# Performance work log

Measured on AMD Instinct MI355X. Metric: run time of the kernel, lower is better.

## Reference

```python
import jax, jax.numpy as jnp
import numpy as np

B, N, C = 4, 4096, 1024
NUM_HEADS = 16
HEAD_DIM = C // NUM_HEADS


def setup_inputs() -> dict:
    key = jax.random.key(0)
    k1, k2, k3, k4 = jax.random.split(key, 4)
    s_in = 1.0 / np.sqrt(C)
    return {
        "x": jax.random.normal(k1, (B, N, C), dtype=jnp.float32),
        "H": 64,
        "W": 64,
        "Wqkv": jax.random.normal(k2, (3 * C, C), dtype=jnp.float32) * s_in,
        "Wproj": jax.random.normal(k3, (C, C), dtype=jnp.float32) * s_in,
        "bproj": jnp.zeros((C,), dtype=jnp.float32),
        "alpha": jnp.ones((NUM_HEADS,), dtype=jnp.float32),
    }


def reference(x, H, W, Wqkv, Wproj, bproj, alpha):
    Bb, Nn, Cc = x.shape
    h, d = NUM_HEADS, HEAD_DIM
    # qkv: [B, N, 3C] -> [3, B, h, N, d]
    qkv = jnp.einsum('bnc,oc->bno', x, Wqkv)
    qkv = qkv.reshape(Bb, Nn, 3, h, d).transpose(2, 0, 3, 1, 4)
    q, k, v = qkv[0], qkv[1], qkv[2]  # each [B, h, N, d]
    # channel attention: contract over tokens N -> [B, h, d, d]
    attn = jnp.einsum('bhnd,bhne->bhde', k, q) / alpha[None, :, None, None]
    attn = jax.nn.softmax(attn, axis=-1)
    # (dropout is identity in eval/reference mode)
    # head_out: [B, h, d, N] -> transpose -> [B, N, h, d] -> concat heads
    out = jnp.einsum('bhde,bhne->bhdn', attn, v)
    out = out.transpose(0, 3, 1, 2).reshape(Bb, Nn, Cc)
    return jnp.einsum('bnc,oc->bno', out, Wproj) + bproj
```

## Files before the change

### kernel.cpp

```cpp
#include <hip/hip_runtime.h>
#include <hip/hip_bf16.h>
#include <cstdint>
#include <cstddef>

typedef unsigned short u16;
typedef __bf16 bf16x8 __attribute__((ext_vector_type(8)));
typedef float f32x4 __attribute__((ext_vector_type(4)));
typedef unsigned short u16x4 __attribute__((ext_vector_type(4)));
typedef unsigned short u16x8 __attribute__((ext_vector_type(8)));

#define AS1(p) ((__attribute__((address_space(1))) void*)(p))
#define AS3(p) ((__attribute__((address_space(3))) void*)(p))

__device__ __forceinline__ float bf2f(u16 u) {
  unsigned v = ((unsigned)u) << 16; float f; __builtin_memcpy(&f, &v, 4); return f;
}
__device__ __forceinline__ u16 f2bf(float f) {
  unsigned u; __builtin_memcpy(&u, &f, 4);
  u += 0x7FFFu + ((u >> 16) & 1u);
  return (u16)(u >> 16);
}

__global__ __launch_bounds__(256) void convert_kernel(const float* __restrict__ src,
                                                      u16* __restrict__ dst, int n4) {
  int i = blockIdx.x * blockDim.x + threadIdx.x;
  int stride = gridDim.x * blockDim.x;
  for (; i < n4; i += stride) {
    float4 v = ((const float4*)src)[i];
    u16x4 o;
    o.x = f2bf(v.x); o.y = f2bf(v.y); o.z = f2bf(v.z); o.w = f2bf(v.w);
    ((u16x4*)dst)[i] = o;
  }
}

__global__ __launch_bounds__(256) void convert_split_kernel(const float* __restrict__ src,
                                                            u16* __restrict__ hi,
                                                            u16* __restrict__ lo, int n4) {
  int i = blockIdx.x * blockDim.x + threadIdx.x;
  int stride = gridDim.x * blockDim.x;
  for (; i < n4; i += stride) {
    float4 v = ((const float4*)src)[i];
    u16x4 oh, ol;
    oh.x = f2bf(v.x); ol.x = f2bf(v.x - bf2f(oh.x));
    oh.y = f2bf(v.y); ol.y = f2bf(v.y - bf2f(oh.y));
    oh.z = f2bf(v.z); ol.z = f2bf(v.z - bf2f(oh.z));
    oh.w = f2bf(v.w); ol.w = f2bf(v.w - bf2f(oh.w));
    ((u16x4*)hi)[i] = oh;
    ((u16x4*)lo)[i] = ol;
  }
}

__global__ __launch_bounds__(256) void transpose_split_kernel(const float* __restrict__ x,
                                                              u16* __restrict__ Xb,
                                                              u16* __restrict__ XThi,
                                                              u16* __restrict__ XTlo) {
  __shared__ u16 lhi[64 * 72];
  __shared__ u16 llo[64 * 72];
  const int t  = threadIdx.x;
  const int nT = blockIdx.x, cT = blockIdx.y, b = blockIdx.z;
  const size_t xbase = ((size_t)b * 4096 + nT * 64) * 1024 + cT * 64;
  const int c4 = (t & 15) * 4;
  const int r0 = t >> 4;
  const int rot_w = (t & 3) << 4;
#pragma unroll
  for (int j = 0; j < 4; ++j) {
    int r = r0 + j * 16;
    float4 v = *(const float4*)(x + xbase + (size_t)r * 1024 + c4);
    u16x4 hi;
    hi.x = f2bf(v.x); hi.y = f2bf(v.y); hi.z = f2bf(v.z); hi.w = f2bf(v.w);
    *(u16x4*)(Xb + xbase + (size_t)r * 1024 + c4) = hi;
    u16 lo[4];
    lo[0] = f2bf(v.x - bf2f(hi.x)); lo[1] = f2bf(v.y - bf2f(hi.y));
    lo[2] = f2bf(v.z - bf2f(hi.z)); lo[3] = f2bf(v.w - bf2f(hi.w));
    u16 hia[4] = { hi.x, hi.y, hi.z, hi.w };
    const int rs = r ^ rot_w;
#pragma unroll
    for (int i = 0; i < 4; ++i) {
      lhi[(c4 + i) * 72 + rs] = hia[i];
      llo[(c4 + i) * 72 + rs] = lo[i];
    }
  }
  __syncthreads();
  const int c  = t >> 2;
  const int n0 = (t & 3) * 16;
  const int rot_r = ((t >> 4) & 3) << 4;
  const int nA = n0 ^ rot_r;
  const size_t tbase = ((size_t)b * 1024 + cT * 64 + c) * 4096 + nT * 64 + n0;
  *(u16x8*)(XThi + tbase)     = *(const u16x8*)(lhi + c * 72 + nA);
  *(u16x8*)(XThi + tbase + 8) = *(const u16x8*)(lhi + c * 72 + nA + 8);
  *(u16x8*)(XTlo + tbase)     = *(const u16x8*)(llo + c * 72 + nA);
  *(u16x8*)(XTlo + tbase + 8) = *(const u16x8*)(llo + c * 72 + nA + 8);
}

template<bool OUT_BF16, bool HAS_BIAS>
__global__ __launch_bounds__(512, 2) void gemm_pipe(const u16* __restrict__ A,
                                                    const u16* __restrict__ B,
                                                    void* __restrict__ Cv,
                                                    const float* __restrict__ bias,
                                                    int M, int N, int K,
                                                    size_t sA, size_t sB, size_t sC) {
  __shared__ __align__(16) u16 lds[4][2][8192];
  const int tid  = threadIdx.x;
  const int lane = tid & 63;
  const int wave = tid >> 6;
  const int wm = wave >> 2, wn = wave & 3;
  const int rowTile = blockIdx.x * 256;
  const int colTile = blockIdx.y * 256;
  A += (size_t)blockIdx.z * sA;
  B += (size_t)blockIdx.z * sB;

  size_t srcA[2], srcB[2];
  int ldsOff[2];
#pragma unroll
  for (int j = 0; j < 2; ++j) {
    const int L = j * 512 + tid;
    const int sr = L >> 3;
    const int slot = (L & 7) ^ (sr & 7);
    const int r  = (sr << 1) | (slot >> 2);
    const int kq = slot & 3;
    srcA[j] = (size_t)(rowTile + r) * K + kq * 8;
    srcB[j] = (size_t)(colTile + r) * K + kq * 8;
    ldsOff[j] = (j * 512 + (tid & 448)) * 16;
  }

  const int m15 = lane & 15, kq4 = lane >> 4;
  const int r0a = wm * 128 + m15, sa0 = r0a >> 1;
  const int idxA0 = sa0 * 64 + (((((r0a & 1) << 2) | kq4)) ^ (sa0 & 7)) * 8;
  const int r0b = wn * 64 + m15, sb0 = r0b >> 1;
  const int idxB0 = sb0 * 64 + (((((r0b & 1) << 2) | kq4)) ^ (sb0 & 7)) * 8;

  const int NT = K >> 5;

  auto stageA = [&](int tt) {
    char* d = (char*)&lds[tt & 3][0][0];
    const int kt = tt << 5;
#pragma unroll
    for (int j = 0; j < 2; ++j)
      __builtin_amdgcn_global_load_lds(AS1(A + srcA[j] + kt), AS3(d + ldsOff[j]), 16, 0, 0);
  };
  auto stageB = [&](int tt) {
    char* d = (char*)&lds[tt & 3][1][0];
    const int kt = tt << 5;
#pragma unroll
    for (int j = 0; j < 2; ++j)
      __builtin_amdgcn_global_load_lds(AS1(B + srcB[j] + kt), AS3(d + ldsOff[j]), 16, 0, 0);
  };

  stageA(0); stageB(0);
  if (NT > 1) { stageA(1); stageB(1); }
  if (NT > 2) { stageA(2); stageB(2); }
  if (NT > 2) asm volatile("s_waitcnt vmcnt(8)" ::: "memory");
  else        asm volatile("s_waitcnt vmcnt(0)" ::: "memory");
  __builtin_amdgcn_sched_barrier(0);
  __builtin_amdgcn_s_barrier();
  __builtin_amdgcn_sched_barrier(0);

  f32x4 acc[8][4] = {};
  for (int t = 0; t < NT; ++t) {
    const u16* bufA = &lds[t & 3][0][0];
    const u16* bufB = &lds[t & 3][1][0];
    bf16x8 a[8], bfr[4];
#pragma unroll
    for (int ni = 0; ni < 4; ++ni) bfr[ni] = *(const bf16x8*)(bufB + idxB0 + ni * 512);
#pragma unroll
    for (int mi = 0; mi < 4; ++mi) a[mi] = *(const bf16x8*)(bufA + idxA0 + mi * 512);
    if (t + 3 < NT) stageA(t + 3);
    __builtin_amdgcn_sched_barrier(0);
    __builtin_amdgcn_s_barrier();
    __builtin_amdgcn_sched_barrier(0);
    __builtin_amdgcn_s_setprio(1);
#pragma unroll
    for (int mi = 0; mi < 4; ++mi)
#pragma unroll
      for (int ni = 0; ni < 4; ++ni)
        acc[mi][ni] = __builtin_amdgcn_mfma_f32_16x16x32_bf16(a[mi], bfr[ni], acc[mi][ni], 0, 0, 0);
    __builtin_amdgcn_s_setprio(0);
    __builtin_amdgcn_sched_barrier(0);
    __builtin_amdgcn_s_barrier();
    __builtin_amdgcn_sched_barrier(0);
#pragma unroll
    for (int mi = 4; mi < 8; ++mi) a[mi] = *(const bf16x8*)(bufA + idxA0 + mi * 512);
    if (t + 3 < NT) stageB(t + 3);
    __builtin_amdgcn_sched_barrier(0);
    __builtin_amdgcn_s_barrier();
    __builtin_amdgcn_sched_barrier(0);
    __builtin_amdgcn_s_setprio(1);
#pragma unroll
    for (int mi = 4; mi < 8; ++mi)
#pragma unroll
      for (int ni = 0; ni < 4; ++ni)
        acc[mi][ni] = __builtin_amdgcn_mfma_f32_16x16x32_bf16(a[mi], bfr[ni], acc[mi][ni], 0, 0, 0);
    __builtin_amdgcn_s_setprio(0);
    if (t < NT - 1) {
      if (t + 3 < NT)      asm volatile("s_waitcnt vmcnt(8)" ::: "memory");
      else if (t + 2 < NT) asm volatile("s_waitcnt vmcnt(4)" ::: "memory");
      else                 asm volatile("s_waitcnt vmcnt(0)" ::: "memory");
    }
    __builtin_amdgcn_sched_barrier(0);
    __builtin_amdgcn_s_barrier();
    __builtin_amdgcn_sched_barrier(0);
  }

  const int crow0 = rowTile + wm * 128 + (lane >> 4) * 4;
  const int ccol0 = colTile + wn * 64 + m15;
  if constexpr (OUT_BF16) {
    u16* C = (u16*)Cv + (size_t)blockIdx.z * sC;
#pragma unroll
    for (int mi = 0; mi < 8; ++mi)
#pragma unroll
      for (int ni = 0; ni < 4; ++ni) {
        const int col = ccol0 + ni * 16;
        const float bv = HAS_BIAS ? bias[col] : 0.f;
#pragma unroll
        for (int r = 0; r < 4; ++r)
          C[(size_t)(crow0 + mi * 16 + r) * N + col] = f2bf(acc[mi][ni][r] + bv);
      }
  } else {
    float* C = (float*)Cv + (size_t)blockIdx.z * sC;
#pragma unroll
    for (int mi = 0; mi < 8; ++mi)
#pragma unroll
      for (int ni = 0; ni < 4; ++ni) {
        const int col = ccol0 + ni * 16;
        const float bv = HAS_BIAS ? bias[col] : 0.f;
#pragma unroll
        for (int r = 0; r < 4; ++r)
          C[(size_t)(crow0 + mi * 16 + r) * N + col] = acc[mi][ni][r] + bv;
      }
  }
}

template<int L>
__device__ __forceinline__ void pipe4_core(const u16* __restrict__ pAh,
                                           const u16* __restrict__ pAl,
                                           const u16* __restrict__ pBh,
                                           const u16* __restrict__ pBl,
                                           u16* lds, int ldsByteOff,
                                           int idxA0, int idxB0, int bOff, int NT,
                                           f32x4 acc[4][2]) {
  auto stage2A = [&](int tt) {
    u16* d = lds + (tt & 3) * 16384;
    const int kt = tt << 5;
    __builtin_amdgcn_global_load_lds(AS1(pAh + kt), AS3((char*)d + ldsByteOff), 16, 0, 0);
    __builtin_amdgcn_global_load_lds(AS1(pAl + kt), AS3((char*)(d + 4096) + ldsByteOff), 16, 0, 0);
  };
  auto stage2B = [&](int tt) {
    if constexpr (L == 4) {
      u16* d = lds + (tt & 3) * 16384 + 8192;
      const int kt = tt << 5;
      __builtin_amdgcn_global_load_lds(AS1(pBh + kt), AS3((char*)d + ldsByteOff), 16, 0, 0);
      __builtin_amdgcn_global_load_lds(AS1(pBl + kt), AS3((char*)(d + 4096) + ldsByteOff), 16, 0, 0);
    }
  };

  stage2A(0); stage2B(0);
  stage2A(1); stage2B(1);
  stage2A(2); stage2B(2);
  if constexpr (L == 4) asm volatile("s_waitcnt vmcnt(8)" ::: "memory");
  else                  asm volatile("s_waitcnt vmcnt(4)" ::: "memory");
  __builtin_amdgcn_sched_barrier(0);
  __builtin_amdgcn_s_barrier();
  __builtin_amdgcn_sched_barrier(0);

  for (int t = 0; t < NT; ++t) {
    const u16* base = lds + (t & 3) * 16384;
    bf16x8 ah[4], al[4], bh[2], bl[2];
    bh[0] = *(const bf16x8*)(base + bOff + idxB0);
    bh[1] = *(const bf16x8*)(base + bOff + idxB0 + 512);
    bl[0] = *(const bf16x8*)(base + bOff + 4096 + idxB0);
    bl[1] = *(const bf16x8*)(base + bOff + 4096 + idxB0 + 512);
    ah[0] = *(const bf16x8*)(base + idxA0);
    ah[1] = *(const bf16x8*)(base + idxA0 + 512);
    al[0] = *(const bf16x8*)(base + 4096 + idxA0);
    al[1] = *(const bf16x8*)(base + 4096 + idxA0 + 512);
    if (t + 3 < NT) stage2A(t + 3);
    __builtin_amdgcn_sched_barrier(0);
    __builtin_amdgcn_s_barrier();
    __builtin_amdgcn_sched_barrier(0);
    __builtin_amdgcn_s_setprio(1);
#pragma unroll
    for (int mi = 0; mi < 2; ++mi)
#pragma unroll
      for (int ni = 0; ni < 2; ++ni) {
        acc[mi][ni] = __builtin_amdgcn_mfma_f32_16x16x32_bf16(ah[mi], bh[ni], acc[mi][ni], 0, 0, 0);
        acc[mi][ni] = __builtin_amdgcn_mfma_f32_16x16x32_bf16(ah[mi], bl[ni], acc[mi][ni], 0, 0, 0);
        acc[mi][ni] = __builtin_amdgcn_mfma_f32_16x16x32_bf16(al[mi], bh[ni], acc[mi][ni], 0, 0, 0);
      }
    __builtin_amdgcn_s_setprio(0);
    __builtin_amdgcn_sched_barrier(0);
    __builtin_amdgcn_s_barrier();
    __builtin_amdgcn_sched_barrier(0);
    ah[2] = *(const bf16x8*)(base + idxA0 + 1024);
    ah[3] = *(const bf16x8*)(base + idxA0 + 1536);
    al[2] = *(const bf16x8*)(base + 4096 + idxA0 + 1024);
    al[3] = *(const bf16x8*)(base + 4096 + idxA0 + 1536);
    if (t + 3 < NT) stage2B(t + 3);
    __builtin_amdgcn_sched_barrier(0);
    __builtin_amdgcn_s_barrier();
    __builtin_amdgcn_sched_barrier(0);
    __builtin_amdgcn_s_setprio(1);
#pragma unroll
    for (int mi = 2; mi < 4; ++mi)
#pragma unroll
      for (int ni = 0; ni < 2; ++ni) {
        acc[mi][ni] = __builtin_amdgcn_mfma_f32_16x16x32_bf16(ah[mi], bh[ni], acc[mi][ni], 0, 0, 0);
        acc[mi][ni] = __builtin_amdgcn_mfma_f32_16x16x32_bf16(ah[mi], bl[ni], acc[mi][ni], 0, 0, 0);
        acc[mi][ni] = __builtin_amdgcn_mfma_f32_16x16x32_bf16(al[mi], bh[ni], acc[mi][ni], 0, 0, 0);
      }
    __builtin_amdgcn_s_setprio(0);
    if (t < NT - 1) {
      if constexpr (L == 4) {
        if (t + 3 < NT)      asm volatile("s_waitcnt vmcnt(8)" ::: "memory");
        else if (t + 2 < NT) asm volatile("s_waitcnt vmcnt(4)" ::: "memory");
        else                 asm volatile("s_waitcnt vmcnt(0)" ::: "memory");
      } else {
        if (t + 3 < NT)      asm volatile("s_waitcnt vmcnt(4)" ::: "memory");
        else if (t + 2 < NT) asm volatile("s_waitcnt vmcnt(2)" ::: "memory");
        else                 asm volatile("s_waitcnt vmcnt(0)" ::: "memory");
      }
    }
    __builtin_amdgcn_sched_barrier(0);
    __builtin_amdgcn_s_barrier();
    __builtin_amdgcn_sched_barrier(0);
  }
}

template<int L>
__device__ __forceinline__ void pipe4k_core(const u16* __restrict__ pAh,
                                            const u16* __restrict__ pAl,
                                            const u16* __restrict__ pBh,
                                            const u16* __restrict__ pBl,
                                            u16* lds, int ldsByteOff,
                                            int idxA0, int idxB0, int bOff,
                                            int NT, int half,
                                            f32x4 acc[4][4]) {
  auto stage = [&](int tt) {
    u16* d = lds + (tt & 3) * 16384;
    const int kt = tt << 5;
    __builtin_amdgcn_global_load_lds(AS1(pAh + kt), AS3((char*)d + ldsByteOff), 16, 0, 0);
    __builtin_amdgcn_global_load_lds(AS1(pAl + kt), AS3((char*)(d + 4096) + ldsByteOff), 16, 0, 0);
    if constexpr (L == 4) {
      __builtin_amdgcn_global_load_lds(AS1(pBh + kt), AS3((char*)(d + 8192) + ldsByteOff), 16, 0, 0);
      __builtin_amdgcn_global_load_lds(AS1(pBl + kt), AS3((char*)(d + 12288) + ldsByteOff), 16, 0, 0);
    }
  };

  stage(0); stage(1); stage(2); stage(3);
  if constexpr (L == 4) asm volatile("s_waitcnt vmcnt(8)" ::: "memory");
  else                  asm volatile("s_waitcnt vmcnt(4)" ::: "memory");
  __builtin_amdgcn_sched_barrier(0);
  __builtin_amdgcn_s_barrier();
  __builtin_amdgcn_sched_barrier(0);

  const int npairs = NT >> 1;
  for (int i = 0; i < npairs; ++i) {
    const u16* base = lds + ((2 * i + half) & 3) * 16384;
    bf16x8 ah[4], al[4], bh[4], bl[4];
#pragma unroll
    for (int ni = 0; ni < 4; ++ni) {
      bh[ni] = *(const bf16x8*)(base + bOff + idxB0 + ni * 512);
      bl[ni] = *(const bf16x8*)(base + bOff + 4096 + idxB0 + ni * 512);
    }
    ah[0] = *(const bf16x8*)(base + idxA0);
    ah[1] = *(const bf16x8*)(base + idxA0 + 512);
    al[0] = *(const bf16x8*)(base + 4096 + idxA0);
    al[1] = *(const bf16x8*)(base + 4096 + idxA0 + 512);
    __builtin_amdgcn_sched_barrier(0);
    __builtin_amdgcn_s_barrier();
    __builtin_amdgcn_sched_barrier(0);
    __builtin_amdgcn_s_setprio(1);
#pragma unroll
    for (int mi = 0; mi < 2; ++mi)
#pragma unroll
      for (int ni = 0; ni < 4; ++ni) {
        acc[mi][ni] = __builtin_amdgcn_mfma_f32_16x16x32_bf16(ah[mi], bh[ni], acc[mi][ni], 0, 0, 0);
        acc[mi][ni] = __builtin_amdgcn_mfma_f32_16x16x32_bf16(ah[mi], bl[ni], acc[mi][ni], 0, 0, 0);
        acc[mi][ni] = __builtin_amdgcn_mfma_f32_16x16x32_bf16(al[mi], bh[ni], acc[mi][ni], 0, 0, 0);
      }
    __builtin_amdgcn_s_setprio(0);
    __builtin_amdgcn_sched_barrier(0);
    __builtin_amdgcn_s_barrier();
    __builtin_amdgcn_sched_barrier(0);
    ah[2] = *(const bf16x8*)(base + idxA0 + 1024);
    ah[3] = *(const bf16x8*)(base + idxA0 + 1536);
    al[2] = *(const bf16x8*)(base + 4096 + idxA0 + 1024);
    al[3] = *(const bf16x8*)(base + 4096 + idxA0 + 1536);
    __builtin_amdgcn_sched_barrier(0);
    __builtin_amdgcn_s_barrier();
    __builtin_amdgcn_sched_barrier(0);
    if (i + 2 < npairs) { stage(2 * i + 4); stage(2 * i + 5); }
    __builtin_amdgcn_sched_barrier(0);
    __builtin_amdgcn_s_setprio(1);
#pragma unroll
    for (int mi = 2; mi < 4; ++mi)
#pragma unroll
      for (int ni = 0; ni < 4; ++ni) {
        acc[mi][ni] = __builtin_amdgcn_mfma_f32_16x16x32_bf16(ah[mi], bh[ni], acc[mi][ni], 0, 0, 0);
        acc[mi][ni] = __builtin_amdgcn_mfma_f32_16x16x32_bf16(ah[mi], bl[ni], acc[mi][ni], 0, 0, 0);
        acc[mi][ni] = __builtin_amdgcn_mfma_f32_16x16x32_bf16(al[mi], bh[ni], acc[mi][ni], 0, 0, 0);
      }
    __builtin_amdgcn_s_setprio(0);
    if (i < npairs - 1) {
      if (i + 2 < npairs) {
        if constexpr (L == 4) asm volatile("s_waitcnt vmcnt(8)" ::: "memory");
        else                  asm volatile("s_waitcnt vmcnt(4)" ::: "memory");
      } else {
        asm volatile("s_waitcnt vmcnt(0)" ::: "memory");
      }
    }
    __builtin_amdgcn_sched_barrier(0);
    __builtin_amdgcn_s_barrier();
    __builtin_amdgcn_sched_barrier(0);
  }
}

__global__ __launch_bounds__(512, 2) void gram_pipe(const u16* __restrict__ XThi,
                                                    const u16* __restrict__ XTlo,
                                                    float* __restrict__ Gpart) {
  __shared__ __align__(16) u16 ldsmem[4 * 4 * 4096];
  const int tid = threadIdx.x, lane = tid & 63, wave = tid >> 6;
  const int q = wave & 3, half = wave >> 2;
  const int qm = q >> 1, qn = q & 1;
  const int bid = blockIdx.x;
  int b, rT, cT, slice, k0, NT; bool same = false;
  if (bid < 64) {
    b = bid & 3; const int j2 = bid >> 2;
    rT = cT = j2 >> 1; slice = j2 & 1; k0 = slice * 2048; NT = 64; same = true;
  } else {
    const int e = bid - 64; b = e & 3;
    const int idx = e >> 2; const int tile = idx >> 2, kq = idx & 3;
    int t = tile, rt = 0;
    while (t >= 7 - rt) { t -= 7 - rt; ++rt; }
    const int ct = rt + 1 + t;
    rT = rt; cT = ct;
    if (kq >= 2) { rT = ct; cT = rt; }
    slice = kq & 1; k0 = kq * 1024; NT = 32;
  }
  const int rowTile = rT * 128, colTile = cT * 128;
  const u16* Ah = XThi + ((size_t)b << 22);
  const u16* Al = XTlo + ((size_t)b << 22);

  const int sr = tid >> 3;
  const int slot = (tid & 7) ^ (sr & 7);
  const int r = (sr << 1) | (slot >> 2);
  const int kq8 = (slot & 3) * 8;
  const u16* pAh = Ah + (size_t)(rowTile + r) * 4096 + k0 + kq8;
  const u16* pAl = Al + (size_t)(rowTile + r) * 4096 + k0 + kq8;
  const u16* pBh = Ah + (size_t)(colTile + r) * 4096 + k0 + kq8;
  const u16* pBl = Al + (size_t)(colTile + r) * 4096 + k0 + kq8;
  const int ldsByteOff = (tid & 448) * 16;

  const int m15 = lane & 15, kq4 = lane >> 4;
  const int r0a = qm * 64 + m15, sa0 = r0a >> 1;
  const int idxA0 = sa0 * 64 + (((((r0a & 1) << 2) | kq4)) ^ (sa0 & 7)) * 8;
  const int r0b = qn * 64 + m15, sb0 = r0b >> 1;
  const int idxB0 = sb0 * 64 + (((((r0b & 1) << 2) | kq4)) ^ (sb0 & 7)) * 8;

  f32x4 acc[4][4] = {};
  if (same) pipe4k_core<2>(pAh, pAl, pAh, pAl, ldsmem, ldsByteOff, idxA0, idxB0, 0, NT, half, acc);
  else      pipe4k_core<4>(pAh, pAl, pBh, pBl, ldsmem, ldsByteOff, idxA0, idxB0, 8192, NT, half, acc);

  float* red = (float*)ldsmem;
  const int rr = (lane >> 4) * 4;
  if (half) {
#pragma unroll
    for (int mi = 0; mi < 4; ++mi)
#pragma unroll
      for (int ni = 0; ni < 4; ++ni)
        *(f32x4*)(red + q * 4352 + (ni * 16 + m15) * 68 + mi * 16 + rr) = acc[mi][ni];
  }
  __syncthreads();
  if (!half) {
    float* out = Gpart + ((size_t)(slice * 4 + b) << 20);
    const int crow0 = rowTile + qm * 64 + rr;
    const int ccol0 = colTile + qn * 64 + m15;
#pragma unroll
    for (int mi = 0; mi < 4; ++mi)
#pragma unroll
      for (int ni = 0; ni < 4; ++ni) {
        f32x4 v = *(const f32x4*)(red + q * 4352 + (ni * 16 + m15) * 68 + mi * 16 + rr);
        v += acc[mi][ni];
#pragma unroll
        for (int r4 = 0; r4 < 4; ++r4)
          out[(size_t)(crow0 + mi * 16 + r4) * 1024 + ccol0 + ni * 16] = v[r4];
      }
  }
}

__global__ __launch_bounds__(256) void gram_reduce_split(const float* __restrict__ Gp,
                                                         u16* __restrict__ Ghi,
                                                         u16* __restrict__ Glo) {
  const int rt = blockIdx.x, ct = blockIdx.y, b = blockIdx.z;
  const bool diag128 = (rt >> 1) == (ct >> 1);
  const float* s0 = Gp + ((size_t)b << 20);
  const float* s1 = Gp + ((size_t)(4 + b) << 20);
  __shared__ float lT[64 * 68];
  const int t = threadIdx.x;
  const int r = t >> 2;
  const int c16 = (t & 3) * 16;

  if (!diag128) {
    const size_t bb = (size_t)(ct * 64 + r) * 1024 + rt * 64 + c16;
#pragma unroll
    for (int q = 0; q < 4; ++q) {
      float4 v0 = *(const float4*)(s0 + bb + q * 4);
      float4 v1 = *(const float4*)(s1 + bb + q * 4);
      float4 s = { v0.x + v1.x, v0.y + v1.y, v0.z + v1.z, v0.w + v1.w };
      *(float4*)(lT + r * 68 + c16 + q * 4) = s;
    }
    __syncthreads();
  }

  const size_t ab = (size_t)(rt * 64 + r) * 1024 + ct * 64 + c16;
  const size_t ob = ((size_t)b << 20) + ab;
#pragma unroll
  for (int q = 0; q < 4; ++q) {
    float4 v0 = *(const float4*)(s0 + ab + q * 4);
    float4 v1 = *(const float4*)(s1 + ab + q * 4);
    float g[4] = { v0.x + v1.x, v0.y + v1.y, v0.z + v1.z, v0.w + v1.w };
    if (!diag128) {
#pragma unroll
      for (int i = 0; i < 4; ++i) g[i] += lT[(c16 + q * 4 + i) * 68 + r];
    }
    u16x4 oh, ol;
    oh.x = f2bf(g[0]); ol.x = f2bf(g[0] - bf2f(oh.x));
    oh.y = f2bf(g[1]); ol.y = f2bf(g[1] - bf2f(oh.y));
    oh.z = f2bf(g[2]); ol.z = f2bf(g[2] - bf2f(oh.z));
    oh.w = f2bf(g[3]); ol.w = f2bf(g[3] - bf2f(oh.w));
    *(u16x4*)(Ghi + ob + q * 4) = oh;
    *(u16x4*)(Glo + ob + q * 4) = ol;
  }
}

__global__ __launch_bounds__(512, 2) void tprime_pipe(const u16* __restrict__ Wqh,
                                                      const u16* __restrict__ Wql,
                                                      const u16* __restrict__ Ghi,
                                                      const u16* __restrict__ Glo,
                                                      u16* __restrict__ Tph,
                                                      u16* __restrict__ Tpl) {
  __shared__ __align__(16) u16 lds[4 * 4 * 4096];
  const int tid = threadIdx.x, lane = tid & 63, wave = tid >> 6;
  const int wm = wave >> 2, wn = wave & 3;
  const int bid = blockIdx.x;
  const int b = bid & 3, tile = bid >> 2;
  const int rowTile = (tile >> 3) * 128, colTile = (tile & 7) * 128;
  const size_t zoff = (size_t)b << 20;

  const int sr = tid >> 3;
  const int slot = (tid & 7) ^ (sr & 7);
  const int r = (sr << 1) | (slot >> 2);
  const int kq8 = (slot & 3) * 8;
  const u16* pAh = Wqh + (size_t)(rowTile + r) * 1024 + kq8;
  const u16* pAl = Wql + (size_t)(rowTile + r) * 1024 + kq8;
  const u16* pBh = Ghi + zoff + (size_t)(colTile + r) * 1024 + kq8;
  const u16* pBl = Glo + zoff + (size_t)(colTile + r) * 1024 + kq8;
  const int ldsByteOff = (tid & 448) * 16;

  const int m15 = lane & 15, kq4 = lane >> 4;
  const int r0a = wm * 64 + m15, sa0 = r0a >> 1;
  const int idxA0 = sa0 * 64 + (((((r0a & 1) << 2) | kq4)) ^ (sa0 & 7)) * 8;
  const int r0b = wn * 32 + m15, sb0 = r0b >> 1;
  const int idxB0 = sb0 * 64 + (((((r0b & 1) << 2) | kq4)) ^ (sb0 & 7)) * 8;

  f32x4 acc[4][2] = {};
  pipe4_core<4>(pAh, pAl, pBh, pBl, lds, ldsByteOff, idxA0, idxB0, 8192, 32, acc);

  const int crow0 = rowTile + wm * 64 + (lane >> 4) * 4;
  const int ccol0 = colTile + wn * 32 + m15;
#pragma unroll
  for (int mi = 0; mi < 4; ++mi)
#pragma unroll
    for (int ni = 0; ni < 2; ++ni)
#pragma unroll
      for (int r4 = 0; r4 < 4; ++r4) {
        float v = acc[mi][ni][r4];
        u16 hi = f2bf(v);
        u16 lo = f2bf(v - bf2f(hi));
        size_t off = zoff + (size_t)(crow0 + mi * 16 + r4) * 1024 + ccol0 + ni * 16;
        Tph[off] = hi;
        Tpl[off] = lo;
      }
}

__global__ __launch_bounds__(512) void s_softmax_kernel(const u16* __restrict__ Wqh,
                                                        const u16* __restrict__ Wql,
                                                        const u16* __restrict__ Tph,
                                                        const u16* __restrict__ Tpl,
                                                        const float* __restrict__ alpha,
                                                        u16* __restrict__ attnT) {
  const int h = blockIdx.x, b = blockIdx.y;
  const int tid = threadIdx.x, lane = tid & 63, wave = tid >> 6;
  const int half = wave >> 2, w4 = wave & 3;
  __shared__ __align__(16) u16 sm[2][4][64 * 32];

  const size_t aBase = (size_t)(1024 + h * 64) * 1024;
  const size_t bBase = ((size_t)b << 20) + (size_t)(h * 64) * 1024;

  const int tid2 = tid & 255;
  const int sr = tid2 >> 3;
  const int slot = (tid2 & 7) ^ (sr & 7);
  const int r = (sr << 1) | (slot >> 2);
  const int kq8 = (slot & 3) * 8;
  const u16* pAh = Wqh + aBase + (size_t)r * 1024 + kq8;
  const u16* pAl = Wql + aBase + (size_t)r * 1024 + kq8;
  const u16* pBh = Tph + bBase + (size_t)r * 1024 + kq8;
  const u16* pBl = Tpl + bBase + (size_t)r * 1024 + kq8;
  const int off = (tid2 & 192) * 16;

  const int m = lane & 15, kq4 = lane >> 4;
  const int rA = w4 * 16 + m, sA0 = rA >> 1;
  const int idxA = sA0 * 64 + (((((rA & 1) << 2) | kq4)) ^ (sA0 & 7)) * 8;
  int idxB[4];
#pragma unroll
  for (int cb = 0; cb < 4; ++cb) {
    const int rB = cb * 16 + m, sB0 = rB >> 1;
    idxB[cb] = sB0 * 64 + (((((rB & 1) << 2) | kq4)) ^ (sB0 & 7)) * 8;
  }

  f32x4 acc[4] = {};
  for (int i = 0; i < 16; ++i) {
    const int kt = (2 * i + half) * 32;
    __builtin_amdgcn_global_load_lds(AS1(pAh + kt), AS3((char*)&sm[half][0][0] + off), 16, 0, 0);
    __builtin_amdgcn_global_load_lds(AS1(pAl + kt), AS3((char*)&sm[half][1][0] + off), 16, 0, 0);
    __builtin_amdgcn_global_load_lds(AS1(pBh + kt), AS3((char*)&sm[half][2][0] + off), 16, 0, 0);
    __builtin_amdgcn_global_load_lds(AS1(pBl + kt), AS3((char*)&sm[half][3][0] + off), 16, 0, 0);
    __syncthreads();
    bf16x8 ah = *(const bf16x8*)(&sm[half][0][0] + idxA);
    bf16x8 al = *(const bf16x8*)(&sm[half][1][0] + idxA);
#pragma unroll
    for (int cb = 0; cb < 4; ++cb) {
      bf16x8 bh = *(const bf16x8*)(&sm[half][2][0] + idxB[cb]);
      bf16x8 bl = *(const bf16x8*)(&sm[half][3][0] + idxB[cb]);
      acc[cb] = __builtin_amdgcn_mfma_f32_16x16x32_bf16(ah, bh, acc[cb], 0, 0, 0);
      acc[cb] = __builtin_amdgcn_mfma_f32_16x16x32_bf16(ah, bl, acc[cb], 0, 0, 0);
      acc[cb] = __builtin_amdgcn_mfma_f32_16x16x32_bf16(al, bh, acc[cb], 0, 0, 0);
    }
    __syncthreads();
  }

  float* red = (float*)&sm[0][0][0];
  const int rbase = (w4 * 64 + lane) * 20;
  if (half) {
#pragma unroll
    for (int cb = 0; cb < 4; ++cb)
      *(f32x4*)(red + rbase + cb * 4) = acc[cb];
  }
  __syncthreads();
  if (!half) {
#pragma unroll
    for (int cb = 0; cb < 4; ++cb)
      acc[cb] += *(const f32x4*)(red + rbase + cb * 4);

    const float invA = 1.f / alpha[h];
    const int g = lane >> 4;
    const size_t obase = (size_t)(b * 16 + h) * 4096;
#pragma unroll
    for (int rr = 0; rr < 4; ++rr) {
      int d = w4 * 16 + g * 4 + rr;
      float s[4];
#pragma unroll
      for (int cb = 0; cb < 4; ++cb) s[cb] = acc[cb][rr] * invA;
      float mx = fmaxf(fmaxf(s[0], s[1]), fmaxf(s[2], s[3]));
#pragma unroll
      for (int o = 1; o < 16; o <<= 1) mx = fmaxf(mx, __shfl_xor(mx, o, 64));
      float e[4]; float sum = 0.f;
#pragma unroll
      for (int cb = 0; cb < 4; ++cb) { e[cb] = __expf(s[cb] - mx); sum += e[cb]; }
#pragma unroll
      for (int o = 1; o < 16; o <<= 1) sum += __shfl_xor(sum, o, 64);
      float inv = 1.f / sum;
#pragma unroll
      for (int cb = 0; cb < 4; ++cb) {
        int e_idx = cb * 16 + (lane & 15);
        attnT[obase + (size_t)e_idx * 64 + d] = f2bf(e[cb] * inv);
      }
    }
  }
}

__global__ __launch_bounds__(256) void m_build_kernel(const u16* __restrict__ Wpb,
                                                      const u16* __restrict__ attnT,
                                                      u16* __restrict__ Mb) {
  const int oT = blockIdx.x, h = blockIdx.y, b = blockIdx.z;
  const int tid = threadIdx.x, lane = tid & 63, wave = tid >> 6;
  __shared__ __align__(16) u16 lA[128 * 64];
  __shared__ __align__(16) u16 lB[64 * 64];
  const int bh = b * 16 + h;
#pragma unroll
  for (int i = 0; i < 4; ++i) {
    int idx = i * 256 + tid;
    int row = idx >> 3;
    int kc  = (idx & 7) * 8;
    int ldsOff = (i * 256 + (tid & 192)) * 16;
    __builtin_amdgcn_global_load_lds(AS1(Wpb + (size_t)(oT * 128 + row) * 1024 + h * 64 + kc),
                                     AS3((char*)lA + ldsOff), 16, 0, 0);
  }
#pragma unroll
  for (int i = 0; i < 2; ++i) {
    int idx = i * 256 + tid;
    int ldsOff = (i * 256 + (tid & 192)) * 16;
    __builtin_amdgcn_global_load_lds(AS1(attnT + (size_t)bh * 4096 + idx * 8),
                                     AS3((char*)lB + ldsOff), 16, 0, 0);
  }
  __syncthreads();
  const int m  = lane & 15;
  const int ko = (lane >> 4) * 8;
  const int wr = wave * 32;
  f32x4 acc[2][4] = {};
#pragma unroll
  for (int ks = 0; ks < 2; ++ks) {
#pragma unroll
    for (int rb = 0; rb < 2; ++rb) {
      bf16x8 a = *(const bf16x8*)(lA + (wr + rb * 16 + m) * 64 + ks * 32 + ko);
#pragma unroll
      for (int cb = 0; cb < 4; ++cb) {
        bf16x8 bb = *(const bf16x8*)(lB + (cb * 16 + m) * 64 + ks * 32 + ko);
        acc[rb][cb] = __builtin_amdgcn_mfma_f32_16x16x32_bf16(a, bb, acc[rb][cb], 0, 0, 0);
      }
    }
  }
  u16* out = Mb + ((size_t)b << 20);
#pragma unroll
  for (int rb = 0; rb < 2; ++rb)
#pragma unroll
    for (int cb = 0; cb < 4; ++cb) {
      int col = h * 64 + cb * 16 + (lane & 15);
#pragma unroll
      for (int r = 0; r < 4; ++r) {
        int row = oT * 128 + wr + rb * 16 + (lane >> 4) * 4 + r;
        out[(size_t)row * 1024 + col] = f2bf(acc[rb][cb][r]);
      }
    }
}

extern "C" void kernel_launch(void* const* d_in, const int* in_sizes, int n_in,
                              void* d_out, int out_size, void* d_ws, size_t ws_size,
                              hipStream_t stream) {
  const float* x     = (const float*)d_in[0];
  const float* Wqkv  = (const float*)d_in[3];
  const float* Wproj = (const float*)d_in[4];
  const float* bproj = (const float*)d_in[5];
  const float* alpha = (const float*)d_in[6];

  char* ws = (char*)d_ws;
  u16*   Xb     = (u16*)ws;
  float* Gpart  = (float*)ws;
  u16*   Mb     = (u16*)ws;
  u16*   XThi   = (u16*)(ws + 33554432);
  u16*   attnTb = (u16*)(ws + 33554432);
  u16*   XTlo  = (u16*)(ws + 67108864);
  u16*   Ghi   = (u16*)(ws + 67108864);
  u16*   Glo   = (u16*)(ws + 75497472);
  u16*   Tph   = (u16*)(ws + 83886080);
  u16*   Tpl   = (u16*)(ws + 92274688);
  u16*   Wqh   = (u16*)(ws + 100663296);
  u16*   Wql   = (u16*)(ws + 106954752);
  u16*   Vb    = (u16*)(ws + 113246208);
  u16*   Wpb   = (u16*)(ws + 146800640);

  transpose_split_kernel<<<dim3(64, 16, 4), 256, 0, stream>>>(x, Xb, XThi, XTlo);
  convert_split_kernel<<<256, 256, 0, stream>>>(Wqkv, Wqh, Wql, 3145728 / 4);
  convert_kernel<<<128, 256, 0, stream>>>(Wproj, Wpb, 1048576 / 4);
  gemm_pipe<true, false><<<dim3(64, 4, 1), 512, 0, stream>>>(
      Xb, Wqh + (size_t)2048 * 1024, Vb, nullptr, 16384, 1024, 1024,
      (size_t)0, (size_t)0, (size_t)0);
  gram_pipe<<<dim3(512), 512, 0, stream>>>(XThi, XTlo, Gpart);
  gram_reduce_split<<<dim3(16, 16, 4), 256, 0, stream>>>(Gpart, Ghi, Glo);
  tprime_pipe<<<dim3(256), 512, 0, stream>>>(Wqh, Wql, Ghi, Glo, Tph, Tpl);
  s_softmax_kernel<<<dim3(16, 4), 512, 0, stream>>>(Wqh, Wql, Tph, Tpl, alpha, attnTb);
  m_build_kernel<<<dim3(8, 16, 4), 256, 0, stream>>>(Wpb, attnTb, Mb);
  gemm_pipe<false, true><<<dim3(16, 4, 4), 512, 0, stream>>>(
      Vb, Mb, (float*)d_out, bproj, 4096, 1024, 1024,
      (size_t)1 << 22, (size_t)1 << 20, (size_t)1 << 22);
}
```

Measured before the change: 369.0 us.

## Stream-K balance gram kernel with atomic accumulation into single partial buffer

Replaces the fixed per-block tile/k-slice assignment in the Gram kernel with a stream-K style split: each of 256 blocks processes a contiguous range of 72 k-iterations across the 36 upper-triangular tiles, possibly spanning tile boundaries. Partial results are accumulated with float atomicAdd into one zeroed Gram buffer, so the reduce kernel reads a single buffer instead of summing two slices. This aims to even out load across CUs and halve the grid to one wave of blocks. It adds a memset, atomic traffic and nondeterministic summation order.

```diff
diff --git a/kernel.cpp b/kernel.cpp
--- a/kernel.cpp
+++ b/kernel.cpp
@@ -421,33 +421,15 @@
   const int tid = threadIdx.x, lane = tid & 63, wave = tid >> 6;
   const int q = wave & 3, half = wave >> 2;
   const int qm = q >> 1, qn = q & 1;
-  const int bid = blockIdx.x;
-  int b, rT, cT, slice, k0, NT; bool same = false;
-  if (bid < 64) {
-    b = bid & 3; const int j2 = bid >> 2;
-    rT = cT = j2 >> 1; slice = j2 & 1; k0 = slice * 2048; NT = 64; same = true;
-  } else {
-    const int e = bid - 64; b = e & 3;
-    const int idx = e >> 2; const int tile = idx >> 2, kq = idx & 3;
-    int t = tile, rt = 0;
-    while (t >= 7 - rt) { t -= 7 - rt; ++rt; }
-    const int ct = rt + 1 + t;
-    rT = rt; cT = ct;
-    if (kq >= 2) { rT = ct; cT = rt; }
-    slice = kq & 1; k0 = kq * 1024; NT = 32;
-  }
-  const int rowTile = rT * 128, colTile = cT * 128;
+  const int b = blockIdx.x & 3, j = blockIdx.x >> 2;
   const u16* Ah = XThi + ((size_t)b << 22);
   const u16* Al = XTlo + ((size_t)b << 22);
+  float* out = Gpart + ((size_t)b << 20);
 
   const int sr = tid >> 3;
   const int slot = (tid & 7) ^ (sr & 7);
   const int r = (sr << 1) | (slot >> 2);
   const int kq8 = (slot & 3) * 8;
-  const u16* pAh = Ah + (size_t)(rowTile + r) * 4096 + k0 + kq8;
-  const u16* pAl = Al + (size_t)(rowTile + r) * 4096 + k0 + kq8;
-  const u16* pBh = Ah + (size_t)(colTile + r) * 4096 + k0 + kq8;
-  const u16* pBl = Al + (size_t)(colTile + r) * 4096 + k0 + kq8;
   const int ldsByteOff = (tid & 448) * 16;
 
   const int m15 = lane & 15, kq4 = lane >> 4;
@@ -455,35 +437,53 @@
   const int idxA0 = sa0 * 64 + (((((r0a & 1) << 2) | kq4)) ^ (sa0 & 7)) * 8;
   const int r0b = qn * 64 + m15, sb0 = r0b >> 1;
   const int idxB0 = sb0 * 64 + (((((r0b & 1) << 2) | kq4)) ^ (sb0 & 7)) * 8;
-
-  f32x4 acc[4][4] = {};
-  if (same) pipe4k_core<2>(pAh, pAl, pAh, pAl, ldsmem, ldsByteOff, idxA0, idxB0, 0, NT, half, acc);
-  else      pipe4k_core<4>(pAh, pAl, pBh, pBl, ldsmem, ldsByteOff, idxA0, idxB0, 8192, NT, half, acc);
-
-  float* red = (float*)ldsmem;
   const int rr = (lane >> 4) * 4;
-  if (half) {
-#pragma unroll
-    for (int mi = 0; mi < 4; ++mi)
-#pragma unroll
-      for (int ni = 0; ni < 4; ++ni)
-        *(f32x4*)(red + q * 4352 + (ni * 16 + m15) * 68 + mi * 16 + rr) = acc[mi][ni];
-  }
-  __syncthreads();
-  if (!half) {
-    float* out = Gpart + ((size_t)(slice * 4 + b) << 20);
-    const int crow0 = rowTile + qm * 64 + rr;
-    const int ccol0 = colTile + qn * 64 + m15;
-#pragma unroll
-    for (int mi = 0; mi < 4; ++mi)
-#pragma unroll
-      for (int ni = 0; ni < 4; ++ni) {
-        f32x4 v = *(const f32x4*)(red + q * 4352 + (ni * 16 + m15) * 68 + mi * 16 + rr);
-        v += acc[mi][ni];
-#pragma unroll
-        for (int r4 = 0; r4 < 4; ++r4)
-          out[(size_t)(crow0 + mi * 16 + r4) * 1024 + ccol0 + ni * 16] = v[r4];
-      }
+
+  int u0 = j * 72;
+  const int u1 = u0 + 72;
+  while (u0 < u1) {
+    const int tile = u0 >> 7;
+    const int ks = u0 & 127;
+    int len = 128 - ks;
+    if (u0 + len > u1) len = u1 - u0;
+    int t2 = tile, rt = 0;
+    while (t2 >= 8 - rt) { t2 -= 8 - rt; ++rt; }
+    const int ct = rt + t2;
+    const int rowTile = rt * 128, colTile = ct * 128;
+    const int k0 = ks * 32;
+    const u16* pAh = Ah + (size_t)(rowTile + r) * 4096 + k0 + kq8;
+    const u16* pAl = Al + (size_t)(rowTile + r) * 4096 + k0 + kq8;
+    const u16* pBh = Ah + (size_t)(colTile + r) * 4096 + k0 + kq8;
+    const u16* pBl = Al + (size_t)(colTile + r) * 4096 + k0 + kq8;
+
+    f32x4 acc[4][4] = {};
+    pipe4k_core<4>(pAh, pAl, pBh, pBl, ldsmem, ldsByteOff, idxA0, idxB0, 8192, len, half, acc);
+
+    float* red = (float*)ldsmem;
+    if (half) {
+#pragma unroll
+      for (int mi = 0; mi < 4; ++mi)
+#pragma unroll
+        for (int ni = 0; ni < 4; ++ni)
+          *(f32x4*)(red + q * 4352 + (ni * 16 + m15) * 68 + mi * 16 + rr) = acc[mi][ni];
+    }
+    __syncthreads();
+    if (!half) {
+      const int crow0 = rowTile + qm * 64 + rr;
+      const int ccol0 = colTile + qn * 64 + m15;
+#pragma unroll
+      for (int mi = 0; mi < 4; ++mi)
+#pragma unroll
+        for (int ni = 0; ni < 4; ++ni) {
+          f32x4 v = *(const f32x4*)(red + q * 4352 + (ni * 16 + m15) * 68 + mi * 16 + rr);
+          v += acc[mi][ni];
+#pragma unroll
+          for (int r4 = 0; r4 < 4; ++r4)
+            atomicAdd(&out[(size_t)(crow0 + mi * 16 + r4) * 1024 + ccol0 + ni * 16], v[r4]);
+        }
+    }
+    __syncthreads();
+    u0 += len;
   }
 }
 
@@ -493,7 +493,6 @@
   const int rt = blockIdx.x, ct = blockIdx.y, b = blockIdx.z;
   const bool diag128 = (rt >> 1) == (ct >> 1);
   const float* s0 = Gp + ((size_t)b << 20);
-  const float* s1 = Gp + ((size_t)(4 + b) << 20);
   __shared__ float lT[64 * 68];
   const int t = threadIdx.x;
   const int r = t >> 2;
@@ -502,12 +501,8 @@
   if (!diag128) {
     const size_t bb = (size_t)(ct * 64 + r) * 1024 + rt * 64 + c16;
 #pragma unroll
-    for (int q = 0; q < 4; ++q) {
-      float4 v0 = *(const float4*)(s0 + bb + q * 4);
-      float4 v1 = *(const float4*)(s1 + bb + q * 4);
-      float4 s = { v0.x + v1.x, v0.y + v1.y, v0.z + v1.z, v0.w + v1.w };
-      *(float4*)(lT + r * 68 + c16 + q * 4) = s;
-    }
+    for (int q = 0; q < 4; ++q)
+      *(float4*)(lT + r * 68 + c16 + q * 4) = *(const float4*)(s0 + bb + q * 4);
     __syncthreads();
   }
 
@@ -516,8 +511,7 @@
 #pragma unroll
   for (int q = 0; q < 4; ++q) {
     float4 v0 = *(const float4*)(s0 + ab + q * 4);
-    float4 v1 = *(const float4*)(s1 + ab + q * 4);
-    float g[4] = { v0.x + v1.x, v0.y + v1.y, v0.z + v1.z, v0.w + v1.w };
+    float g[4] = { v0.x, v0.y, v0.z, v0.w };
     if (!diag128) {
 #pragma unroll
       for (int i = 0; i < 4; ++i) g[i] += lT[(c16 + q * 4 + i) * 68 + r];
@@ -764,7 +758,8 @@
   gemm_pipe<true, false><<<dim3(64, 4, 1), 512, 0, stream>>>(
       Xb, Wqh + (size_t)2048 * 1024, Vb, nullptr, 16384, 1024, 1024,
       (size_t)0, (size_t)0, (size_t)0);
-  gram_pipe<<<dim3(512), 512, 0, stream>>>(XThi, XTlo, Gpart);
+  hipMemsetAsync(Gpart, 0, (size_t)16777216, stream);
+  gram_pipe<<<dim3(256), 512, 0, stream>>>(XThi, XTlo, Gpart);
   gram_reduce_split<<<dim3(16, 16, 4), 256, 0, stream>>>(Gpart, Ghi, Glo);
   tprime_pipe<<<dim3(256), 512, 0, stream>>>(Wqh, Wql, Ghi, Glo, Tph, Tpl);
   s_softmax_kernel<<<dim3(16, 4), 512, 0, stream>>>(Wqh, Wql, Tph, Tpl, alpha, attnTb);
```

After: 381.7 us. +3.4%, slower.
